# Optimization experiments

Hardware: AMD Instinct MI355X
Metric: run time of the kernel (lower is better)

The kernel has to match this reference:

```python
import jax, jax.numpy as jnp
import numpy as np

N_NODES = 100000
N_EDGES = 1250000
D_IN = 64
D_H = 64
D_OUT = 32


def setup_inputs() -> dict:
    key = jax.random.key(0)
    ks = jax.random.split(key, 8)
    x = jax.random.normal(ks[0], (N_NODES, D_IN), dtype=jnp.float32)
    edge_index = jax.random.randint(ks[1], (2, N_EDGES), 0, N_NODES, dtype=jnp.int64)
    s = 0.1
    W1_l = jax.random.normal(ks[2], (D_H, D_IN), dtype=jnp.float32) * s
    W1_r = jax.random.normal(ks[3], (D_H, D_IN), dtype=jnp.float32) * s
    b1 = jnp.zeros((D_H,), dtype=jnp.float32)
    W2_l = jax.random.normal(ks[4], (D_OUT, D_H), dtype=jnp.float32) * s
    W2_r = jax.random.normal(ks[5], (D_OUT, D_H), dtype=jnp.float32) * s
    b2 = jnp.zeros((D_OUT,), dtype=jnp.float32)
    return {"x": x, "edge_index": edge_index, "W1_l": W1_l, "W1_r": W1_r,
            "b1": b1, "W2_l": W2_l, "W2_r": W2_r, "b2": b2}


def _sage_conv(x, src, dst, W_l, W_r, b):
    # PyG SAGEConv (aggr='mean', root_weight=True):
    #   out = lin_l(mean_{j in N(i)} x_j) + lin_r(x_i)
    n = x.shape[0]
    msg = x[src]                                            # [E, d] gather
    ssum = jax.ops.segment_sum(msg, dst, num_segments=n)    # [N, d]
    deg = jax.ops.segment_sum(jnp.ones((src.shape[0], 1), x.dtype), dst,
                              num_segments=n)               # [N, 1]
    mean = ssum / jnp.maximum(deg, 1.0)
    return mean @ W_l.T + b + x @ W_r.T


def reference(x, edge_index, W1_l, W1_r, b1, W2_l, W2_r, b2):
    src = edge_index[0]
    dst = edge_index[1]
    h = jax.nn.relu(_sage_conv(x, src, dst, W1_l, W1_r, b1))
    out = _sage_conv(h, src, dst, W2_l, W2_r, b2)
    return out
```

## Files before the change

### kernel.cpp

```cpp
#include <hip/hip_runtime.h>

#define N_NODES 100000
#define N_EDGES 1250000
#define D_IN 64
#define D_H 64
#define D_OUT 32

#define BUCKETS 196
#define GRP 512
#define PREP_NB 512
#define PREP_CH 2442
#define SCAP 48
#define BSTRIDE (PREP_NB*SCAP)
#define CSRCAP 8192

typedef __attribute__((ext_vector_type(8))) short bf16x8;
typedef __attribute__((ext_vector_type(4))) float f32x4;

__device__ __forceinline__ unsigned short f2bf(float f) {
    unsigned u = __float_as_uint(f);
    u = (u + 0x7fffu + ((u >> 16) & 1u)) >> 16;
    return (unsigned short)u;
}
__device__ __forceinline__ float bfhi(unsigned v) { return __uint_as_float(v & 0xffff0000u); }
__device__ __forceinline__ float bflo(unsigned v) { return __uint_as_float(v << 16); }


__global__ __launch_bounds__(256) void k_prep(const float* __restrict__ x,
                                              unsigned short* __restrict__ xh,
                                              const int* __restrict__ src,
                                              const int* __restrict__ dst,
                                              int* __restrict__ ebuf,
                                              int* __restrict__ pcnt) {
    __shared__ int ofs[BUCKETS];
    int t = threadIdx.x, b = blockIdx.x;
    for (int i = t; i < BUCKETS; i += 256) ofs[i] = 0;
    __syncthreads();

    const int TOT = N_NODES * 64 / 4;
    for (int i = b * 256 + t; i < TOT; i += PREP_NB * 256) {
        float4 v = *(const float4*)(x + (size_t)i * 4);
        uint2 u;
        u.x = (unsigned)f2bf(v.x) | ((unsigned)f2bf(v.y) << 16);
        u.y = (unsigned)f2bf(v.z) | ((unsigned)f2bf(v.w) << 16);
        *(uint2*)(xh + (size_t)i * 4) = u;
    }

    int e0 = b * PREP_CH;
    int e1 = e0 + PREP_CH; if (e1 > N_EDGES) e1 = N_EDGES;
    for (int e = e0 + t; e < e1; e += 256) {
        int s = src[e], d = dst[e];
        if ((unsigned)d >= N_NODES) continue;
        int sv = ((unsigned)s < N_NODES) ? s : 0;
        int bk = d >> 9;
        int r = atomicAdd(&ofs[bk], 1);
        if (r < SCAP) ebuf[bk * BSTRIDE + b * SCAP + r] = ((d & 511) << 17) | sv;
    }
    __syncthreads();
    for (int i = t; i < BUCKETS; i += 256) {
        int v = ofs[i]; if (v > SCAP) v = SCAP;
        pcnt[i * PREP_NB + b] = v;
    }
}

__global__ __launch_bounds__(512) void k_phb(const int* __restrict__ ebuf,
                                             const int* __restrict__ pcnt,
                                             int2* __restrict__ rd,
                                             int* __restrict__ csr_src) {
    __shared__ int sedge[CSRCAP];
    __shared__ int cnt[GRP];
    __shared__ int wsum[8];
    int b = blockIdx.x, t = threadIdx.x;
    int lane = t & 63, w = t >> 6;

    cnt[t] = 0;
    int c = pcnt[b * PREP_NB + t];

    int run = c;
    #pragma unroll
    for (int off = 1; off < 64; off <<= 1) {
        int u = __shfl_up(run, off, 64);
        if (lane >= off) run += u;
    }
    if (lane == 63) wsum[w] = run;
    __syncthreads();
    int wbase = 0, tot = 0;
    #pragma unroll
    for (int i = 0; i < 8; ++i) { int v = wsum[i]; tot += v; if (i < w) wbase += v; }
    int base = wbase + run - c;
    int n = tot; if (n > CSRCAP) n = CSRCAP;

    {
        const int4* sp4 = (const int4*)(ebuf + (size_t)b * BSTRIDE + (size_t)t * SCAP);
        for (int j = 0; j < c; j += 4) {
            int4 v = sp4[j >> 2];
            int p = base + j;
            if (p + 0 < CSRCAP)          sedge[p + 0] = v.x;
            if (j + 1 < c && p + 1 < CSRCAP) sedge[p + 1] = v.y;
            if (j + 2 < c && p + 2 < CSRCAP) sedge[p + 2] = v.z;
            if (j + 3 < c && p + 3 < CSRCAP) sedge[p + 3] = v.w;
        }
    }
    __syncthreads();
    for (int i = t; i < n; i += 512) atomicAdd(&cnt[sedge[i] >> 17], 1);
    __syncthreads();

    int d = cnt[t];
    int rund = d;
    #pragma unroll
    for (int off = 1; off < 64; off <<= 1) {
        int u = __shfl_up(rund, off, 64);
        if (lane >= off) rund += u;
    }
    if (lane == 63) wsum[w] = rund;
    __syncthreads();
    int wb2 = 0;
    #pragma unroll
    for (int i = 0; i < 8; ++i) { if (i < w) wb2 += wsum[i]; }
    int gabs = b * CSRCAP + wb2 + rund - d;
    int node = b * GRP + t;
    if (node < N_NODES) rd[node] = make_int2(gabs, d);
    cnt[t] = gabs;
    __syncthreads();
    for (int i = t; i < n; i += 512) {
        int v = sedge[i];
        int pos = atomicAdd(&cnt[v >> 17], 1);
        csr_src[pos] = v & 0x1FFFF;
    }
}

__global__ __launch_bounds__(256) void k_gather1(
    const unsigned short* __restrict__ xh,
    const int2* __restrict__ rd,
    const int* __restrict__ csr_src,
    unsigned int* __restrict__ meanh)
{
    int lane = threadIdx.x & 63;
    int wv = threadIdx.x >> 6;
    int c = lane & 31;
    int hb = lane & 32;
    const unsigned* xp = (const unsigned*)xh;

    int node0 = blockIdx.x * 8 + wv * 2 + (hb >> 5);
    for (int row = node0; row < N_NODES; row += gridDim.x * 8) {
        int2 rdv = rd[row];
        int start = rdv.x, dg = rdv.y;
        int end = start + dg;
        float x0 = 0.f, y0 = 0.f, x1 = 0.f, y1 = 0.f;
        float x2 = 0.f, y2 = 0.f, x3 = 0.f, y3 = 0.f;
        float x4 = 0.f, y4 = 0.f, x5 = 0.f, y5 = 0.f;
        float x6 = 0.f, y6 = 0.f, x7 = 0.f, y7 = 0.f;
        for (int eb = start; eb < end; eb += 32) {
            int nv = end - eb; if (nv > 32) nv = 32;
            int sid = (c < nv) ? csr_src[eb + c] : 0;
            int j = 0;
            for (; j + 8 <= nv; j += 8) {
                int s0 = __shfl(sid, hb + j + 0, 64);
                int s1 = __shfl(sid, hb + j + 1, 64);
                int s2 = __shfl(sid, hb + j + 2, 64);
                int s3 = __shfl(sid, hb + j + 3, 64);
                int s4 = __shfl(sid, hb + j + 4, 64);
                int s5 = __shfl(sid, hb + j + 5, 64);
                int s6 = __shfl(sid, hb + j + 6, 64);
                int s7 = __shfl(sid, hb + j + 7, 64);
                unsigned v0 = xp[s0 * 32 + c];
                unsigned v1 = xp[s1 * 32 + c];
                unsigned v2 = xp[s2 * 32 + c];
                unsigned v3 = xp[s3 * 32 + c];
                unsigned v4 = xp[s4 * 32 + c];
                unsigned v5 = xp[s5 * 32 + c];
                unsigned v6 = xp[s6 * 32 + c];
                unsigned v7 = xp[s7 * 32 + c];
                x0 += bflo(v0); y0 += bfhi(v0);
                x1 += bflo(v1); y1 += bfhi(v1);
                x2 += bflo(v2); y2 += bfhi(v2);
                x3 += bflo(v3); y3 += bfhi(v3);
                x4 += bflo(v4); y4 += bfhi(v4);
                x5 += bflo(v5); y5 += bfhi(v5);
                x6 += bflo(v6); y6 += bfhi(v6);
                x7 += bflo(v7); y7 += bfhi(v7);
            }
            for (; j + 4 <= nv; j += 4) {
                int s0 = __shfl(sid, hb + j + 0, 64);
                int s1 = __shfl(sid, hb + j + 1, 64);
                int s2 = __shfl(sid, hb + j + 2, 64);
                int s3 = __shfl(sid, hb + j + 3, 64);
                unsigned v0 = xp[s0 * 32 + c];
                unsigned v1 = xp[s1 * 32 + c];
                unsigned v2 = xp[s2 * 32 + c];
                unsigned v3 = xp[s3 * 32 + c];
                x0 += bflo(v0); y0 += bfhi(v0);
                x1 += bflo(v1); y1 += bfhi(v1);
                x2 += bflo(v2); y2 += bfhi(v2);
                x3 += bflo(v3); y3 += bfhi(v3);
            }
            for (; j < nv; ++j) {
                int s = __shfl(sid, hb + j, 64);
                unsigned v = xp[s * 32 + c];
                x0 += bflo(v); y0 += bfhi(v);
            }
        }
        float rdeg = 1.0f / fmaxf((float)dg, 1.0f);
        float fx = (((x0 + x1) + (x2 + x3)) + ((x4 + x5) + (x6 + x7))) * rdeg;
        float fy = (((y0 + y1) + (y2 + y3)) + ((y4 + y5) + (y6 + y7))) * rdeg;
        meanh[(size_t)row * 32 + c] = (unsigned)f2bf(fx) | ((unsigned)f2bf(fy) << 16);
    }
}

__global__ __launch_bounds__(256) void k_gemm1(
    const unsigned short* __restrict__ xh, const unsigned short* __restrict__ meanh,
    const float* __restrict__ W1l, const float* __restrict__ W1r,
    const float* __restrict__ b1,
    const float* __restrict__ W2l, const float* __restrict__ W2r,
    unsigned short* __restrict__ hWlh, unsigned short* __restrict__ hrh)
{
    __shared__ short sWB1[4 * 4 * 64 * 8];
    __shared__ short sWB2[2 * 4 * 64 * 8];
    __shared__ short htile[4][16 * 72];

    int tid = threadIdx.x;
    for (int e = tid; e < 1024; e += 256) {
        int kc = e >> 8, nt = (e >> 6) & 3, ln = e & 63;
        int cc = ln & 15, qd = ln >> 4;
        int n = nt * 16 + cc, k0 = kc * 32 + qd * 8;
        const float* sp = (k0 < 64) ? (W1l + n * 64 + k0) : (W1r + n * 64 + (k0 - 64));
        short* dp = sWB1 + e * 8;
        #pragma unroll
        for (int j = 0; j < 8; ++j) dp[j] = (short)f2bf(sp[j]);
    }
    for (int e = tid; e < 512; e += 256) {
        int kc = e >> 8, nt = (e >> 6) & 3, ln = e & 63;
        int cc = ln & 15, qd = ln >> 4;
        int n = nt * 16 + cc, k0 = kc * 32 + qd * 8;
        const float* sp = (n < 32) ? (W2l + n * 64 + k0) : (W2r + (n - 32) * 64 + k0);
        short* dp = sWB2 + e * 8;
        #pragma unroll
        for (int j = 0; j < 8; ++j) dp[j] = (short)f2bf(sp[j]);
    }
    __syncthreads();

    int lane = tid & 63, w = tid >> 6;
    int c = lane & 15, quad = lane >> 4;
    float bias[4];
    #pragma unroll
    for (int nt = 0; nt < 4; ++nt) bias[nt] = b1[nt * 16 + c];

    const bf16x8* B1 = (const bf16x8*)sWB1;
    const bf16x8* B2 = (const bf16x8*)sWB2;
    short* ht = htile[w];

    for (int r0 = blockIdx.x * 64 + w * 16; r0 < N_NODES; r0 += gridDim.x * 64) {
        int ra = r0 + c; if (ra > N_NODES - 1) ra = N_NODES - 1;
        const bf16x8* mrow = (const bf16x8*)(meanh + (size_t)ra * 64);
        const bf16x8* xrow = (const bf16x8*)(xh + (size_t)ra * 64);
        bf16x8 a0 = mrow[quad];
        bf16x8 a1 = mrow[4 + quad];
        bf16x8 a2 = xrow[quad];
        bf16x8 a3 = xrow[4 + quad];

        f32x4 acc[4];
        #pragma unroll
        for (int nt = 0; nt < 4; ++nt) acc[nt] = (f32x4){0.f, 0.f, 0.f, 0.f};
        #pragma unroll
        for (int nt = 0; nt < 4; ++nt)
            acc[nt] = __builtin_amdgcn_mfma_f32_16x16x32_bf16(a0, B1[(0 * 4 + nt) * 64 + lane], acc[nt], 0, 0, 0);
        #pragma unroll
        for (int nt = 0; nt < 4; ++nt)
            acc[nt] = __builtin_amdgcn_mfma_f32_16x16x32_bf16(a1, B1[(1 * 4 + nt) * 64 + lane], acc[nt], 0, 0, 0);
        #pragma unroll
        for (int nt = 0; nt < 4; ++nt)
            acc[nt] = __builtin_amdgcn_mfma_f32_16x16x32_bf16(a2, B1[(2 * 4 + nt) * 64 + lane], acc[nt], 0, 0, 0);
        #pragma unroll
        for (int nt = 0; nt < 4; ++nt)
            acc[nt] = __builtin_amdgcn_mfma_f32_16x16x32_bf16(a3, B1[(3 * 4 + nt) * 64 + lane], acc[nt], 0, 0, 0);

        #pragma unroll
        for (int nt = 0; nt < 4; ++nt) {
            #pragma unroll
            for (int reg = 0; reg < 4; ++reg) {
                float hv = fmaxf(acc[nt][reg] + bias[nt], 0.0f);
                ht[(quad * 4 + reg) * 72 + nt * 16 + c] = (short)f2bf(hv);
            }
        }
        bf16x8 h0 = *(const bf16x8*)(ht + c * 72 + 0  + quad * 8);
        bf16x8 h1 = *(const bf16x8*)(ht + c * 72 + 32 + quad * 8);

        f32x4 acc2[4];
        #pragma unroll
        for (int nt = 0; nt < 4; ++nt) acc2[nt] = (f32x4){0.f, 0.f, 0.f, 0.f};
        #pragma unroll
        for (int nt = 0; nt < 4; ++nt)
            acc2[nt] = __builtin_amdgcn_mfma_f32_16x16x32_bf16(h0, B2[(0 * 4 + nt) * 64 + lane], acc2[nt], 0, 0, 0);
        #pragma unroll
        for (int nt = 0; nt < 4; ++nt)
            acc2[nt] = __builtin_amdgcn_mfma_f32_16x16x32_bf16(h1, B2[(1 * 4 + nt) * 64 + lane], acc2[nt], 0, 0, 0);

        #pragma unroll
        for (int nt = 0; nt < 4; ++nt) {
            #pragma unroll
            for (int reg = 0; reg < 4; ++reg) {
                int row = r0 + quad * 4 + reg;
                if (row < N_NODES) {
                    unsigned short q = f2bf(acc2[nt][reg]);
                    if (nt < 2) hWlh[(size_t)row * 32 + nt * 16 + c] = q;
                    else        hrh [(size_t)row * 32 + (nt - 2) * 16 + c] = q;
                }
            }
        }
    }
}

__global__ __launch_bounds__(256) void k_l2(
    const unsigned short* __restrict__ hWlh, const unsigned short* __restrict__ hrh,
    const int2* __restrict__ rd,
    const int* __restrict__ csr_src,
    const float* __restrict__ b2, float* __restrict__ out)
{
    int lane = threadIdx.x & 63;
    int wv = threadIdx.x >> 6;
    int c = lane & 15;
    int qb = lane & 48;
    const unsigned* hp  = (const unsigned*)hWlh;
    const unsigned* hrp = (const unsigned*)hrh;
    float2 b2v = ((const float2*)b2)[c];

    int node0 = blockIdx.x * 16 + wv * 4 + (qb >> 4);
    for (int row = node0; row < N_NODES; row += gridDim.x * 16) {
        int2 rdv = rd[row];
        int start = rdv.x, dg = rdv.y;
        int end = start + dg;
        float x0 = 0.f, y0 = 0.f, x1 = 0.f, y1 = 0.f;
        float x2 = 0.f, y2 = 0.f, x3 = 0.f, y3 = 0.f;
        float x4 = 0.f, y4 = 0.f, x5 = 0.f, y5 = 0.f;
        float x6 = 0.f, y6 = 0.f, x7 = 0.f, y7 = 0.f;
        for (int eb = start; eb < end; eb += 16) {
            int nv = end - eb; if (nv > 16) nv = 16;
            int sid = (c < nv) ? csr_src[eb + c] : 0;
            int j = 0;
            for (; j + 8 <= nv; j += 8) {
                int s0 = __shfl(sid, qb + j + 0, 64);
                int s1 = __shfl(sid, qb + j + 1, 64);
                int s2 = __shfl(sid, qb + j + 2, 64);
                int s3 = __shfl(sid, qb + j + 3, 64);
                int s4 = __shfl(sid, qb + j + 4, 64);
                int s5 = __shfl(sid, qb + j + 5, 64);
                int s6 = __shfl(sid, qb + j + 6, 64);
                int s7 = __shfl(sid, qb + j + 7, 64);
                unsigned v0 = hp[s0 * 16 + c];
                unsigned v1 = hp[s1 * 16 + c];
                unsigned v2 = hp[s2 * 16 + c];
                unsigned v3 = hp[s3 * 16 + c];
                unsigned v4 = hp[s4 * 16 + c];
                unsigned v5 = hp[s5 * 16 + c];
                unsigned v6 = hp[s6 * 16 + c];
                unsigned v7 = hp[s7 * 16 + c];
                x0 += bflo(v0); y0 += bfhi(v0);
                x1 += bflo(v1); y1 += bfhi(v1);
                x2 += bflo(v2); y2 += bfhi(v2);
                x3 += bflo(v3); y3 += bfhi(v3);
                x4 += bflo(v4); y4 += bfhi(v4);
                x5 += bflo(v5); y5 += bfhi(v5);
                x6 += bflo(v6); y6 += bfhi(v6);
                x7 += bflo(v7); y7 += bfhi(v7);
            }
            for (; j + 4 <= nv; j += 4) {
                int s0 = __shfl(sid, qb + j + 0, 64);
                int s1 = __shfl(sid, qb + j + 1, 64);
                int s2 = __shfl(sid, qb + j + 2, 64);
                int s3 = __shfl(sid, qb + j + 3, 64);
                unsigned v0 = hp[s0 * 16 + c];
                unsigned v1 = hp[s1 * 16 + c];
                unsigned v2 = hp[s2 * 16 + c];
                unsigned v3 = hp[s3 * 16 + c];
                x0 += bflo(v0); y0 += bfhi(v0);
                x1 += bflo(v1); y1 += bfhi(v1);
                x2 += bflo(v2); y2 += bfhi(v2);
                x3 += bflo(v3); y3 += bfhi(v3);
            }
            for (; j < nv; ++j) {
                int s = __shfl(sid, qb + j, 64);
                unsigned v = hp[s * 16 + c];
                x0 += bflo(v); y0 += bfhi(v);
            }
        }
        float fx = ((x0 + x1) + (x2 + x3)) + ((x4 + x5) + (x6 + x7));
        float fy = ((y0 + y1) + (y2 + y3)) + ((y4 + y5) + (y6 + y7));
        float rdeg = 1.0f / fmaxf((float)dg, 1.0f);
        unsigned hru = hrp[(size_t)row * 16 + c];
        float2 o;
        o.x = fmaf(fx, rdeg, bflo(hru) + b2v.x);
        o.y = fmaf(fy, rdeg, bfhi(hru) + b2v.y);
        ((float2*)out)[(size_t)row * 16 + c] = o;
    }
}

extern "C" void kernel_launch(void* const* d_in, const int* in_sizes, int n_in,
                              void* d_out, int out_size, void* d_ws, size_t ws_size,
                              hipStream_t stream) {
    const float* x   = (const float*)d_in[0];
    const int*   ei  = (const int*)d_in[1];
    const float* W1l = (const float*)d_in[2];
    const float* W1r = (const float*)d_in[3];
    const float* b1  = (const float*)d_in[4];
    const float* W2l = (const float*)d_in[5];
    const float* W2r = (const float*)d_in[6];
    const float* b2  = (const float*)d_in[7];
    float* out = (float*)d_out;

    const int* src = ei;
    const int* dst = ei + N_EDGES;

    char* w = (char*)d_ws;
    int2* rd     = (int2*)w;  w += sizeof(int2) * (N_NODES + 4);
    int* pcnt    = (int*)w;   w += sizeof(int) * (PREP_NB * BUCKETS);
    int* csr_src = (int*)w;   w += sizeof(int) * (BUCKETS * CSRCAP);
    int* ebuf    = (int*)w;   w += sizeof(int) * ((size_t)BUCKETS * BSTRIDE);
    unsigned short* xh    = (unsigned short*)w; w += sizeof(short) * (size_t)N_NODES * 64;
    unsigned int*   meanh = (unsigned int*)w;   w += sizeof(int)   * (size_t)N_NODES * 32;
    unsigned short* hWlh  = (unsigned short*)w; w += sizeof(short) * (size_t)N_NODES * 32;
    unsigned short* hrh   = (unsigned short*)w;

    k_prep<<<PREP_NB, 256, 0, stream>>>(x, xh, src, dst, ebuf, pcnt);
    k_phb<<<BUCKETS, 512, 0, stream>>>(ebuf, pcnt, rd, csr_src);
    k_gather1<<<4096, 256, 0, stream>>>(xh, rd, csr_src, meanh);
    k_gemm1<<<(N_NODES + 63) / 64, 256, 0, stream>>>(
        xh, (const unsigned short*)meanh, W1l, W1r, b1, W2l, W2r, hWlh, hrh);
    k_l2<<<4096, 256, 0, stream>>>(hWlh, hrh, rd, csr_src, b2, out);
}
```

Before: 195.7 us.

## Sort nodes by degree for gather balance and widen per-lane gather vectors

Adds a degree histogram in k_phb and a new k_dscat kernel that builds a degree-sorted node permutation, so each wave's gather groups process neighbour lists of similar length and divergence is reduced. The layer-1 gather moves from 32 lanes per node with 4-byte loads to 16 lanes per node with 8-byte loads. The layer-2 gather moves from 16 lanes to 8 lanes per node with uint2 loads and float4 stores. Grid sizes change so that each group handles one node. This adds an extra kernel launch and an indirection through perm, and writes to output rows become scattered.

```diff
diff --git a/kernel.cpp b/kernel.cpp
--- a/kernel.cpp
+++ b/kernel.cpp
@@ -14,6 +14,9 @@
 #define BSTRIDE (PREP_NB*SCAP)
 #define CSRCAP 8192
 
+#define G1_BLOCKS 6250
+#define L2_BLOCKS 3125
+
 typedef __attribute__((ext_vector_type(8))) short bf16x8;
 typedef __attribute__((ext_vector_type(4))) float f32x4;
 
@@ -31,10 +34,13 @@
                                               const int* __restrict__ src,
                                               const int* __restrict__ dst,
                                               int* __restrict__ ebuf,
-                                              int* __restrict__ pcnt) {
+                                              int* __restrict__ pcnt,
+                                              int* __restrict__ dcnt,
+                                              int* __restrict__ gofs) {
     __shared__ int ofs[BUCKETS];
     int t = threadIdx.x, b = blockIdx.x;
     for (int i = t; i < BUCKETS; i += 256) ofs[i] = 0;
+    if (b == 0 && t < 256) { dcnt[t] = 0; gofs[t] = 0; }
     __syncthreads();
 
     const int TOT = N_NODES * 64 / 4;
@@ -66,7 +72,8 @@
 __global__ __launch_bounds__(512) void k_phb(const int* __restrict__ ebuf,
                                              const int* __restrict__ pcnt,
                                              int2* __restrict__ rd,
-                                             int* __restrict__ csr_src) {
+                                             int* __restrict__ csr_src,
+                                             int* __restrict__ dcnt) {
     __shared__ int sedge[CSRCAP];
     __shared__ int cnt[GRP];
     __shared__ int wsum[8];
@@ -95,7 +102,7 @@
         for (int j = 0; j < c; j += 4) {
             int4 v = sp4[j >> 2];
             int p = base + j;
-            if (p + 0 < CSRCAP)          sedge[p + 0] = v.x;
+            if (p + 0 < CSRCAP)              sedge[p + 0] = v.x;
             if (j + 1 < c && p + 1 < CSRCAP) sedge[p + 1] = v.y;
             if (j + 2 < c && p + 2 < CSRCAP) sedge[p + 2] = v.z;
             if (j + 3 < c && p + 3 < CSRCAP) sedge[p + 3] = v.w;
@@ -127,212 +134,85 @@
         int pos = atomicAdd(&cnt[v >> 17], 1);
         csr_src[pos] = v & 0x1FFFF;
     }
-}
+    __syncthreads();
+    if (t < 256) sedge[t] = 0;
+    __syncthreads();
+    int dcl = d; if (dcl > 255) dcl = 255;
+    if (node < N_NODES) atomicAdd(&sedge[dcl], 1);
+    __syncthreads();
+    if (t < 256 && sedge[t] > 0) atomicAdd(&dcnt[t], sedge[t]);
+}
+
+__global__ __launch_bounds__(512) void k_dscat(const int2* __restrict__ rd,
+                                               const int* __restrict__ dcnt,
+                                               int* __restrict__ gofs,
+                                               int* __restrict__ perm) {
+    __shared__ int lh[256];
+    __shared__ int lb[256];
+    __shared__ int wpart[4];
+    int t = threadIdx.x, b = blockIdx.x;
+    int lane = t & 63, w = t >> 6;
+    if (t < 256) lh[t] = 0;
+    __syncthreads();
+    int node = b * 512 + t;
+    int dcl = 0;
+    if (node < N_NODES) {
+        dcl = rd[node].y; if (dcl > 255) dcl = 255;
+        atomicAdd(&lh[dcl], 1);
+    }
+    __syncthreads();
+    int v = 0, run = 0;
+    if (t < 256) {
+        v = dcnt[t]; run = v;
+        #pragma unroll
+        for (int off = 1; off < 64; off <<= 1) {
+            int u = __shfl_up(run, off, 64);
+            if (lane >= off) run += u;
+        }
+        if (lane == 63) wpart[w] = run;
+    }
+    __syncthreads();
+    if (t < 256) {
+        int basep = 0;
+        #pragma unroll
+        for (int i = 0; i < 4; ++i) { if (i < w) basep += wpart[i]; }
+        int sb = basep + run - v;
+        int res = (lh[t] > 0) ? atomicAdd(&gofs[t], lh[t]) : 0;
+        lb[t] = sb + res;
+    }
+    __syncthreads();
+    if (t < 256) lh[t] = lb[t];
+    __syncthreads();
+    if (node < N_NODES) {
+        int pos = atomicAdd(&lh[dcl], 1);
+        perm[pos] = node;
+    }
+}
+
+#define ACC(SET, V) sx##SET += bflo(V.x); sy##SET += bfhi(V.x); \
+                    sz##SET += bflo(V.y); sw##SET += bfhi(V.y)
 
 __global__ __launch_bounds__(256) void k_gather1(
     const unsigned short* __restrict__ xh,
     const int2* __restrict__ rd,
     const int* __restrict__ csr_src,
+    const int* __restrict__ perm,
     unsigned int* __restrict__ meanh)
-{
-    int lane = threadIdx.x & 63;
-    int wv = threadIdx.x >> 6;
-    int c = lane & 31;
-    int hb = lane & 32;
-    const unsigned* xp = (const unsigned*)xh;
-
-    int node0 = blockIdx.x * 8 + wv * 2 + (hb >> 5);
-    for (int row = node0; row < N_NODES; row += gridDim.x * 8) {
-        int2 rdv = rd[row];
-        int start = rdv.x, dg = rdv.y;
-        int end = start + dg;
-        float x0 = 0.f, y0 = 0.f, x1 = 0.f, y1 = 0.f;
-        float x2 = 0.f, y2 = 0.f, x3 = 0.f, y3 = 0.f;
-        float x4 = 0.f, y4 = 0.f, x5 = 0.f, y5 = 0.f;
-        float x6 = 0.f, y6 = 0.f, x7 = 0.f, y7 = 0.f;
-        for (int eb = start; eb < end; eb += 32) {
-            int nv = end - eb; if (nv > 32) nv = 32;
-            int sid = (c < nv) ? csr_src[eb + c] : 0;
-            int j = 0;
-            for (; j + 8 <= nv; j += 8) {
-                int s0 = __shfl(sid, hb + j + 0, 64);
-                int s1 = __shfl(sid, hb + j + 1, 64);
-                int s2 = __shfl(sid, hb + j + 2, 64);
-                int s3 = __shfl(sid, hb + j + 3, 64);
-                int s4 = __shfl(sid, hb + j + 4, 64);
-                int s5 = __shfl(sid, hb + j + 5, 64);
-                int s6 = __shfl(sid, hb + j + 6, 64);
-                int s7 = __shfl(sid, hb + j + 7, 64);
-                unsigned v0 = xp[s0 * 32 + c];
-                unsigned v1 = xp[s1 * 32 + c];
-                unsigned v2 = xp[s2 * 32 + c];
-                unsigned v3 = xp[s3 * 32 + c];
-                unsigned v4 = xp[s4 * 32 + c];
-                unsigned v5 = xp[s5 * 32 + c];
-                unsigned v6 = xp[s6 * 32 + c];
-                unsigned v7 = xp[s7 * 32 + c];
-                x0 += bflo(v0); y0 += bfhi(v0);
-                x1 += bflo(v1); y1 += bfhi(v1);
-                x2 += bflo(v2); y2 += bfhi(v2);
-                x3 += bflo(v3); y3 += bfhi(v3);
-                x4 += bflo(v4); y4 += bfhi(v4);
-                x5 += bflo(v5); y5 += bfhi(v5);
-                x6 += bflo(v6); y6 += bfhi(v6);
-                x7 += bflo(v7); y7 += bfhi(v7);
-            }
-            for (; j + 4 <= nv; j += 4) {
-                int s0 = __shfl(sid, hb + j + 0, 64);
-                int s1 = __shfl(sid, hb + j + 1, 64);
-                int s2 = __shfl(sid, hb + j + 2, 64);
-                int s3 = __shfl(sid, hb + j + 3, 64);
-                unsigned v0 = xp[s0 * 32 + c];
-                unsigned v1 = xp[s1 * 32 + c];
-                unsigned v2 = xp[s2 * 32 + c];
-                unsigned v3 = xp[s3 * 32 + c];
-                x0 += bflo(v0); y0 += bfhi(v0);
-                x1 += bflo(v1); y1 += bfhi(v1);
-                x2 += bflo(v2); y2 += bfhi(v2);
-                x3 += bflo(v3); y3 += bfhi(v3);
-            }
-            for (; j < nv; ++j) {
-                int s = __shfl(sid, hb + j, 64);
-                unsigned v = xp[s * 32 + c];
-                x0 += bflo(v); y0 += bfhi(v);
-            }
-        }
-        float rdeg = 1.0f / fmaxf((float)dg, 1.0f);
-        float fx = (((x0 + x1) + (x2 + x3)) + ((x4 + x5) + (x6 + x7))) * rdeg;
-        float fy = (((y0 + y1) + (y2 + y3)) + ((y4 + y5) + (y6 + y7))) * rdeg;
-        meanh[(size_t)row * 32 + c] = (unsigned)f2bf(fx) | ((unsigned)f2bf(fy) << 16);
-    }
-}
-
-__global__ __launch_bounds__(256) void k_gemm1(
-    const unsigned short* __restrict__ xh, const unsigned short* __restrict__ meanh,
-    const float* __restrict__ W1l, const float* __restrict__ W1r,
-    const float* __restrict__ b1,
-    const float* __restrict__ W2l, const float* __restrict__ W2r,
-    unsigned short* __restrict__ hWlh, unsigned short* __restrict__ hrh)
-{
-    __shared__ short sWB1[4 * 4 * 64 * 8];
-    __shared__ short sWB2[2 * 4 * 64 * 8];
-    __shared__ short htile[4][16 * 72];
-
-    int tid = threadIdx.x;
-    for (int e = tid; e < 1024; e += 256) {
-        int kc = e >> 8, nt = (e >> 6) & 3, ln = e & 63;
-        int cc = ln & 15, qd = ln >> 4;
-        int n = nt * 16 + cc, k0 = kc * 32 + qd * 8;
-        const float* sp = (k0 < 64) ? (W1l + n * 64 + k0) : (W1r + n * 64 + (k0 - 64));
-        short* dp = sWB1 + e * 8;
-        #pragma unroll
-        for (int j = 0; j < 8; ++j) dp[j] = (short)f2bf(sp[j]);
-    }
-    for (int e = tid; e < 512; e += 256) {
-        int kc = e >> 8, nt = (e >> 6) & 3, ln = e & 63;
-        int cc = ln & 15, qd = ln >> 4;
-        int n = nt * 16 + cc, k0 = kc * 32 + qd * 8;
-        const float* sp = (n < 32) ? (W2l + n * 64 + k0) : (W2r + (n - 32) * 64 + k0);
-        short* dp = sWB2 + e * 8;
-        #pragma unroll
-        for (int j = 0; j < 8; ++j) dp[j] = (short)f2bf(sp[j]);
-    }
-    __syncthreads();
-
-    int lane = tid & 63, w = tid >> 6;
-    int c = lane & 15, quad = lane >> 4;
-    float bias[4];
-    #pragma unroll
-    for (int nt = 0; nt < 4; ++nt) bias[nt] = b1[nt * 16 + c];
-
-    const bf16x8* B1 = (const bf16x8*)sWB1;
-    const bf16x8* B2 = (const bf16x8*)sWB2;
-    short* ht = htile[w];
-
-    for (int r0 = blockIdx.x * 64 + w * 16; r0 < N_NODES; r0 += gridDim.x * 64) {
-        int ra = r0 + c; if (ra > N_NODES - 1) ra = N_NODES - 1;
-        const bf16x8* mrow = (const bf16x8*)(meanh + (size_t)ra * 64);
-        const bf16x8* xrow = (const bf16x8*)(xh + (size_t)ra * 64);
-        bf16x8 a0 = mrow[quad];
-        bf16x8 a1 = mrow[4 + quad];
-        bf16x8 a2 = xrow[quad];
-        bf16x8 a3 = xrow[4 + quad];
-
-        f32x4 acc[4];
-        #pragma unroll
-        for (int nt = 0; nt < 4; ++nt) acc[nt] = (f32x4){0.f, 0.f, 0.f, 0.f};
-        #pragma unroll
-        for (int nt = 0; nt < 4; ++nt)
-            acc[nt] = __builtin_amdgcn_mfma_f32_16x16x32_bf16(a0, B1[(0 * 4 + nt) * 64 + lane], acc[nt], 0, 0, 0);
-        #pragma unroll
-        for (int nt = 0; nt < 4; ++nt)
-            acc[nt] = __builtin_amdgcn_mfma_f32_16x16x32_bf16(a1, B1[(1 * 4 + nt) * 64 + lane], acc[nt], 0, 0, 0);
-        #pragma unroll
-        for (int nt = 0; nt < 4; ++nt)
-            acc[nt] = __builtin_amdgcn_mfma_f32_16x16x32_bf16(a2, B1[(2 * 4 + nt) * 64 + lane], acc[nt], 0, 0, 0);
-        #pragma unroll
-        for (int nt = 0; nt < 4; ++nt)
-            acc[nt] = __builtin_amdgcn_mfma_f32_16x16x32_bf16(a3, B1[(3 * 4 + nt) * 64 + lane], acc[nt], 0, 0, 0);
-
-        #pragma unroll
-        for (int nt = 0; nt < 4; ++nt) {
-            #pragma unroll
-            for (int reg = 0; reg < 4; ++reg) {
-                float hv = fmaxf(acc[nt][reg] + bias[nt], 0.0f);
-                ht[(quad * 4 + reg) * 72 + nt * 16 + c] = (short)f2bf(hv);
-            }
-        }
-        bf16x8 h0 = *(const bf16x8*)(ht + c * 72 + 0  + quad * 8);
-        bf16x8 h1 = *(const bf16x8*)(ht + c * 72 + 32 + quad * 8);
-
-        f32x4 acc2[4];
-        #pragma unroll
-        for (int nt = 0; nt < 4; ++nt) acc2[nt] = (f32x4){0.f, 0.f, 0.f, 0.f};
-        #pragma unroll
-        for (int nt = 0; nt < 4; ++nt)
-            acc2[nt] = __builtin_amdgcn_mfma_f32_16x16x32_bf16(h0, B2[(0 * 4 + nt) * 64 + lane], acc2[nt], 0, 0, 0);
-        #pragma unroll
-        for (int nt = 0; nt < 4; ++nt)
-            acc2[nt] = __builtin_amdgcn_mfma_f32_16x16x32_bf16(h1, B2[(1 * 4 + nt) * 64 + lane], acc2[nt], 0, 0, 0);
-
-        #pragma unroll
-        for (int nt = 0; nt < 4; ++nt) {
-            #pragma unroll
-            for (int reg = 0; reg < 4; ++reg) {
-                int row = r0 + quad * 4 + reg;
-                if (row < N_NODES) {
-                    unsigned short q = f2bf(acc2[nt][reg]);
-                    if (nt < 2) hWlh[(size_t)row * 32 + nt * 16 + c] = q;
-                    else        hrh [(size_t)row * 32 + (nt - 2) * 16 + c] = q;
-                }
-            }
-        }
-    }
-}
-
-__global__ __launch_bounds__(256) void k_l2(
-    const unsigned short* __restrict__ hWlh, const unsigned short* __restrict__ hrh,
-    const int2* __restrict__ rd,
-    const int* __restrict__ csr_src,
-    const float* __restrict__ b2, float* __restrict__ out)
 {
     int lane = threadIdx.x & 63;
     int wv = threadIdx.x >> 6;
     int c = lane & 15;
     int qb = lane & 48;
-    const unsigned* hp  = (const unsigned*)hWlh;
-    const unsigned* hrp = (const unsigned*)hrh;
-    float2 b2v = ((const float2*)b2)[c];
-
-    int node0 = blockIdx.x * 16 + wv * 4 + (qb >> 4);
-    for (int row = node0; row < N_NODES; row += gridDim.x * 16) {
+    const uint2* xp = (const uint2*)xh;
+
+    int idx0 = blockIdx.x * 16 + wv * 4 + (qb >> 4);
+    for (int idx = idx0; idx < N_NODES; idx += gridDim.x * 16) {
+        int row = perm[idx];
         int2 rdv = rd[row];
         int start = rdv.x, dg = rdv.y;
         int end = start + dg;
-        float x0 = 0.f, y0 = 0.f, x1 = 0.f, y1 = 0.f;
-        float x2 = 0.f, y2 = 0.f, x3 = 0.f, y3 = 0.f;
-        float x4 = 0.f, y4 = 0.f, x5 = 0.f, y5 = 0.f;
-        float x6 = 0.f, y6 = 0.f, x7 = 0.f, y7 = 0.f;
+        float sx0=0,sy0=0,sz0=0,sw0=0, sx1=0,sy1=0,sz1=0,sw1=0;
+        float sx2=0,sy2=0,sz2=0,sw2=0, sx3=0,sy3=0,sz3=0,sw3=0;
         for (int eb = start; eb < end; eb += 16) {
             int nv = end - eb; if (nv > 16) nv = 16;
             int sid = (c < nv) ? csr_src[eb + c] : 0;
@@ -346,51 +226,226 @@
                 int s5 = __shfl(sid, qb + j + 5, 64);
                 int s6 = __shfl(sid, qb + j + 6, 64);
                 int s7 = __shfl(sid, qb + j + 7, 64);
-                unsigned v0 = hp[s0 * 16 + c];
-                unsigned v1 = hp[s1 * 16 + c];
-                unsigned v2 = hp[s2 * 16 + c];
-                unsigned v3 = hp[s3 * 16 + c];
-                unsigned v4 = hp[s4 * 16 + c];
-                unsigned v5 = hp[s5 * 16 + c];
-                unsigned v6 = hp[s6 * 16 + c];
-                unsigned v7 = hp[s7 * 16 + c];
-                x0 += bflo(v0); y0 += bfhi(v0);
-                x1 += bflo(v1); y1 += bfhi(v1);
-                x2 += bflo(v2); y2 += bfhi(v2);
-                x3 += bflo(v3); y3 += bfhi(v3);
-                x4 += bflo(v4); y4 += bfhi(v4);
-                x5 += bflo(v5); y5 += bfhi(v5);
-                x6 += bflo(v6); y6 += bfhi(v6);
-                x7 += bflo(v7); y7 += bfhi(v7);
+                uint2 v0 = xp[(size_t)s0 * 16 + c];
+                uint2 v1 = xp[(size_t)s1 * 16 + c];
+                uint2 v2 = xp[(size_t)s2 * 16 + c];
+                uint2 v3 = xp[(size_t)s3 * 16 + c];
+                uint2 v4 = xp[(size_t)s4 * 16 + c];
+                uint2 v5 = xp[(size_t)s5 * 16 + c];
+                uint2 v6 = xp[(size_t)s6 * 16 + c];
+                uint2 v7 = xp[(size_t)s7 * 16 + c];
+                ACC(0, v0); ACC(1, v1); ACC(2, v2); ACC(3, v3);
+                ACC(0, v4); ACC(1, v5); ACC(2, v6); ACC(3, v7);
             }
             for (; j + 4 <= nv; j += 4) {
                 int s0 = __shfl(sid, qb + j + 0, 64);
                 int s1 = __shfl(sid, qb + j + 1, 64);
                 int s2 = __shfl(sid, qb + j + 2, 64);
                 int s3 = __shfl(sid, qb + j + 3, 64);
-                unsigned v0 = hp[s0 * 16 + c];
-                unsigned v1 = hp[s1 * 16 + c];
-                unsigned v2 = hp[s2 * 16 + c];
-                unsigned v3 = hp[s3 * 16 + c];
-                x0 += bflo(v0); y0 += bfhi(v0);
-                x1 += bflo(v1); y1 += bfhi(v1);
-                x2 += bflo(v2); y2 += bfhi(v2);
-                x3 += bflo(v3); y3 += bfhi(v3);
+                uint2 v0 = xp[(size_t)s0 * 16 + c];
+                uint2 v1 = xp[(size_t)s1 * 16 + c];
+                uint2 v2 = xp[(size_t)s2 * 16 + c];
+                uint2 v3 = xp[(size_t)s3 * 16 + c];
+                ACC(0, v0); ACC(1, v1); ACC(2, v2); ACC(3, v3);
             }
             for (; j < nv; ++j) {
-                int s = __shfl(sid, qb + j, 64);
-                unsigned v = hp[s * 16 + c];
-                x0 += bflo(v); y0 += bfhi(v);
-            }
-        }
-        float fx = ((x0 + x1) + (x2 + x3)) + ((x4 + x5) + (x6 + x7));
-        float fy = ((y0 + y1) + (y2 + y3)) + ((y4 + y5) + (y6 + y7));
+                int s0 = __shfl(sid, qb + j, 64);
+                uint2 v0 = xp[(size_t)s0 * 16 + c];
+                ACC(0, v0);
+            }
+        }
         float rdeg = 1.0f / fmaxf((float)dg, 1.0f);
-        unsigned hru = hrp[(size_t)row * 16 + c];
-        float2 o;
-        o.x = fmaf(fx, rdeg, bflo(hru) + b2v.x);
-        o.y = fmaf(fy, rdeg, bfhi(hru) + b2v.y);
-        ((float2*)out)[(size_t)row * 16 + c] = o;
+        float mx = ((sx0 + sx1) + (sx2 + sx3)) * rdeg;
+        float my = ((sy0 + sy1) + (sy2 + sy3)) * rdeg;
+        float mz = ((sz0 + sz1) + (sz2 + sz3)) * rdeg;
+        float mw = ((sw0 + sw1) + (sw2 + sw3)) * rdeg;
+        uint2 u;
+        u.x = (unsigned)f2bf(mx) | ((unsigned)f2bf(my) << 16);
+        u.y = (unsigned)f2bf(mz) | ((unsigned)f2bf(mw) << 16);
+        ((uint2*)meanh)[(size_t)row * 16 + c] = u;
+    }
+}
+
+__global__ __launch_bounds__(256) void k_gemm1(
+    const unsigned short* __restrict__ xh, const unsigned short* __restrict__ meanh,
+    const float* __restrict__ W1l, const float* __restrict__ W1r,
+    const float* __restrict__ b1,
+    const float* __restrict__ W2l, const float* __restrict__ W2r,
+    unsigned short* __restrict__ hWlh, unsigned short* __restrict__ hrh)
+{
+    __shared__ short sWB1[4 * 4 * 64 * 8];
+    __shared__ short sWB2[2 * 4 * 64 * 8];
+    __shared__ short htile[4][16 * 72];
+
+    int tid = threadIdx.x;
+    for (int e = tid; e < 1024; e += 256) {
+        int kc = e >> 8, nt = (e >> 6) & 3, ln = e & 63;
+        int cc = ln & 15, qd = ln >> 4;
+        int n = nt * 16 + cc, k0 = kc * 32 + qd * 8;
+        const float* sp = (k0 < 64) ? (W1l + n * 64 + k0) : (W1r + n * 64 + (k0 - 64));
+        short* dp = sWB1 + e * 8;
+        #pragma unroll
+        for (int j = 0; j < 8; ++j) dp[j] = (short)f2bf(sp[j]);
+    }
+    for (int e = tid; e < 512; e += 256) {
+        int kc = e >> 8, nt = (e >> 6) & 3, ln = e & 63;
+        int cc = ln & 15, qd = ln >> 4;
+        int n = nt * 16 + cc, k0 = kc * 32 + qd * 8;
+        const float* sp = (n < 32) ? (W2l + n * 64 + k0) : (W2r + (n - 32) * 64 + k0);
+        short* dp = sWB2 + e * 8;
+        #pragma unroll
+        for (int j = 0; j < 8; ++j) dp[j] = (short)f2bf(sp[j]);
+    }
+    __syncthreads();
+
+    int lane = tid & 63, w = tid >> 6;
+    int c = lane & 15, quad = lane >> 4;
+    float bias[4];
+    #pragma unroll
+    for (int nt = 0; nt < 4; ++nt) bias[nt] = b1[nt * 16 + c];
+
+    const bf16x8* B1 = (const bf16x8*)sWB1;
+    const bf16x8* B2 = (const bf16x8*)sWB2;
+    short* ht = htile[w];
+
+    for (int r0 = blockIdx.x * 64 + w * 16; r0 < N_NODES; r0 += gridDim.x * 64) {
+        int ra = r0 + c; if (ra > N_NODES - 1) ra = N_NODES - 1;
+        const bf16x8* mrow = (const bf16x8*)(meanh + (size_t)ra * 64);
+        const bf16x8* xrow = (const bf16x8*)(xh + (size_t)ra * 64);
+        bf16x8 a0 = mrow[quad];
+        bf16x8 a1 = mrow[4 + quad];
+        bf16x8 a2 = xrow[quad];
+        bf16x8 a3 = xrow[4 + quad];
+
+        f32x4 acc[4];
+        #pragma unroll
+        for (int nt = 0; nt < 4; ++nt) acc[nt] = (f32x4){0.f, 0.f, 0.f, 0.f};
+        #pragma unroll
+        for (int nt = 0; nt < 4; ++nt)
+            acc[nt] = __builtin_amdgcn_mfma_f32_16x16x32_bf16(a0, B1[(0 * 4 + nt) * 64 + lane], acc[nt], 0, 0, 0);
+        #pragma unroll
+        for (int nt = 0; nt < 4; ++nt)
+            acc[nt] = __builtin_amdgcn_mfma_f32_16x16x32_bf16(a1, B1[(1 * 4 + nt) * 64 + lane], acc[nt], 0, 0, 0);
+        #pragma unroll
+        for (int nt = 0; nt < 4; ++nt)
+            acc[nt] = __builtin_amdgcn_mfma_f32_16x16x32_bf16(a2, B1[(2 * 4 + nt) * 64 + lane], acc[nt], 0, 0, 0);
+        #pragma unroll
+        for (int nt = 0; nt < 4; ++nt)
+            acc[nt] = __builtin_amdgcn_mfma_f32_16x16x32_bf16(a3, B1[(3 * 4 + nt) * 64 + lane], acc[nt], 0, 0, 0);
+
+        #pragma unroll
+        for (int nt = 0; nt < 4; ++nt) {
+            #pragma unroll
+            for (int reg = 0; reg < 4; ++reg) {
+                float hv = fmaxf(acc[nt][reg] + bias[nt], 0.0f);
+                ht[(quad * 4 + reg) * 72 + nt * 16 + c] = (short)f2bf(hv);
+            }
+        }
+        bf16x8 h0 = *(const bf16x8*)(ht + c * 72 + 0  + quad * 8);
+        bf16x8 h1 = *(const bf16x8*)(ht + c * 72 + 32 + quad * 8);
+
+        f32x4 acc2[4];
+        #pragma unroll
+        for (int nt = 0; nt < 4; ++nt) acc2[nt] = (f32x4){0.f, 0.f, 0.f, 0.f};
+        #pragma unroll
+        for (int nt = 0; nt < 4; ++nt)
+            acc2[nt] = __builtin_amdgcn_mfma_f32_16x16x32_bf16(h0, B2[(0 * 4 + nt) * 64 + lane], acc2[nt], 0, 0, 0);
+        #pragma unroll
+        for (int nt = 0; nt < 4; ++nt)
+            acc2[nt] = __builtin_amdgcn_mfma_f32_16x16x32_bf16(h1, B2[(1 * 4 + nt) * 64 + lane], acc2[nt], 0, 0, 0);
+
+        #pragma unroll
+        for (int nt = 0; nt < 4; ++nt) {
+            #pragma unroll
+            for (int reg = 0; reg < 4; ++reg) {
+                int row = r0 + quad * 4 + reg;
+                if (row < N_NODES) {
+                    unsigned short q = f2bf(acc2[nt][reg]);
+                    if (nt < 2) hWlh[(size_t)row * 32 + nt * 16 + c] = q;
+                    else        hrh [(size_t)row * 32 + (nt - 2) * 16 + c] = q;
+                }
+            }
+        }
+    }
+}
+
+__global__ __launch_bounds__(256) void k_l2(
+    const unsigned short* __restrict__ hWlh, const unsigned short* __restrict__ hrh,
+    const int2* __restrict__ rd,
+    const int* __restrict__ csr_src,
+    const int* __restrict__ perm,
+    const float* __restrict__ b2, float* __restrict__ out)
+{
+    int lane = threadIdx.x & 63;
+    int wv = threadIdx.x >> 6;
+    int c = lane & 7;
+    int gb = lane & 56;
+    const uint2* hp  = (const uint2*)hWlh;
+    const uint2* hrp = (const uint2*)hrh;
+    float4 b2v = ((const float4*)b2)[c];
+
+    int idx0 = blockIdx.x * 32 + wv * 8 + (gb >> 3);
+    for (int idx = idx0; idx < N_NODES; idx += gridDim.x * 32) {
+        int row = perm[idx];
+        int2 rdv = rd[row];
+        int start = rdv.x, dg = rdv.y;
+        int end = start + dg;
+        float sx0=0,sy0=0,sz0=0,sw0=0, sx1=0,sy1=0,sz1=0,sw1=0;
+        float sx2=0,sy2=0,sz2=0,sw2=0, sx3=0,sy3=0,sz3=0,sw3=0;
+        for (int eb = start; eb < end; eb += 8) {
+            int nv = end - eb; if (nv > 8) nv = 8;
+            int sid = (c < nv) ? csr_src[eb + c] : 0;
+            if (nv == 8) {
+                int s0 = __shfl(sid, gb + 0, 64);
+                int s1 = __shfl(sid, gb + 1, 64);
+                int s2 = __shfl(sid, gb + 2, 64);
+                int s3 = __shfl(sid, gb + 3, 64);
+                int s4 = __shfl(sid, gb + 4, 64);
+                int s5 = __shfl(sid, gb + 5, 64);
+                int s6 = __shfl(sid, gb + 6, 64);
+                int s7 = __shfl(sid, gb + 7, 64);
+                uint2 v0 = hp[(size_t)s0 * 8 + c];
+                uint2 v1 = hp[(size_t)s1 * 8 + c];
+                uint2 v2 = hp[(size_t)s2 * 8 + c];
+                uint2 v3 = hp[(size_t)s3 * 8 + c];
+                uint2 v4 = hp[(size_t)s4 * 8 + c];
+                uint2 v5 = hp[(size_t)s5 * 8 + c];
+                uint2 v6 = hp[(size_t)s6 * 8 + c];
+                uint2 v7 = hp[(size_t)s7 * 8 + c];
+                ACC(0, v0); ACC(1, v1); ACC(2, v2); ACC(3, v3);
+                ACC(0, v4); ACC(1, v5); ACC(2, v6); ACC(3, v7);
+            } else {
+                int j = 0;
+                for (; j + 4 <= nv; j += 4) {
+                    int s0 = __shfl(sid, gb + j + 0, 64);
+                    int s1 = __shfl(sid, gb + j + 1, 64);
+                    int s2 = __shfl(sid, gb + j + 2, 64);
+                    int s3 = __shfl(sid, gb + j + 3, 64);
+                    uint2 v0 = hp[(size_t)s0 * 8 + c];
+                    uint2 v1 = hp[(size_t)s1 * 8 + c];
+                    uint2 v2 = hp[(size_t)s2 * 8 + c];
+                    uint2 v3 = hp[(size_t)s3 * 8 + c];
+                    ACC(0, v0); ACC(1, v1); ACC(2, v2); ACC(3, v3);
+                }
+                for (; j < nv; ++j) {
+                    int s0 = __shfl(sid, gb + j, 64);
+                    uint2 v0 = hp[(size_t)s0 * 8 + c];
+                    ACC(0, v0);
+                }
+            }
+        }
+        float fx = (sx0 + sx1) + (sx2 + sx3);
+        float fy = (sy0 + sy1) + (sy2 + sy3);
+        float fz = (sz0 + sz1) + (sz2 + sz3);
+        float fw = (sw0 + sw1) + (sw2 + sw3);
+        float rdeg = 1.0f / fmaxf((float)dg, 1.0f);
+        uint2 hru = hrp[(size_t)row * 8 + c];
+        float4 o;
+        o.x = fmaf(fx, rdeg, bflo(hru.x) + b2v.x);
+        o.y = fmaf(fy, rdeg, bfhi(hru.x) + b2v.y);
+        o.z = fmaf(fz, rdeg, bflo(hru.y) + b2v.z);
+        o.w = fmaf(fw, rdeg, bfhi(hru.y) + b2v.w);
+        ((float4*)out)[(size_t)row * 8 + c] = o;
     }
 }
 
@@ -418,12 +473,16 @@
     unsigned short* xh    = (unsigned short*)w; w += sizeof(short) * (size_t)N_NODES * 64;
     unsigned int*   meanh = (unsigned int*)w;   w += sizeof(int)   * (size_t)N_NODES * 32;
     unsigned short* hWlh  = (unsigned short*)w; w += sizeof(short) * (size_t)N_NODES * 32;
-    unsigned short* hrh   = (unsigned short*)w;
-
-    k_prep<<<PREP_NB, 256, 0, stream>>>(x, xh, src, dst, ebuf, pcnt);
-    k_phb<<<BUCKETS, 512, 0, stream>>>(ebuf, pcnt, rd, csr_src);
-    k_gather1<<<4096, 256, 0, stream>>>(xh, rd, csr_src, meanh);
+    unsigned short* hrh   = (unsigned short*)w; w += sizeof(short) * (size_t)N_NODES * 32;
+    int* dcnt    = (int*)w;   w += sizeof(int) * 256;
+    int* gofs    = (int*)w;   w += sizeof(int) * 256;
+    int* perm    = (int*)w;
+
+    k_prep<<<PREP_NB, 256, 0, stream>>>(x, xh, src, dst, ebuf, pcnt, dcnt, gofs);
+    k_phb<<<BUCKETS, 512, 0, stream>>>(ebuf, pcnt, rd, csr_src, dcnt);
+    k_dscat<<<BUCKETS, 512, 0, stream>>>(rd, dcnt, gofs, perm);
+    k_gather1<<<G1_BLOCKS, 256, 0, stream>>>(xh, rd, csr_src, perm, meanh);
     k_gemm1<<<(N_NODES + 63) / 64, 256, 0, stream>>>(
         xh, (const unsigned short*)meanh, W1l, W1r, b1, W2l, W2r, hWlh, hrh);
-    k_l2<<<4096, 256, 0, stream>>>(hWlh, hrh, rd, csr_src, b2, out);
-}
+    k_l2<<<L2_BLOCKS, 256, 0, stream>>>(hWlh, hrh, rd, csr_src, perm, b2, out);
+}
```

New measurement: 208.0 us. 1.06x slower.
